# Kernel tuning notes

Measured on AMD Instinct MI355X. Metric: run time of the kernel, lower is better.

Reference implementation:

```python
import jax, jax.numpy as jnp
import numpy as np

NUM_NODES = 100000
EMBED_DIM = 64
NUM_LAYERS = 3
NUM_EDGES = 1250000


def setup_inputs() -> dict:
    key = jax.random.key(0)
    k1, k2 = jax.random.split(key)
    edge_index = jax.random.randint(k1, (2, NUM_EDGES), 0, NUM_NODES, dtype=jnp.int64)
    emb_weight = jax.random.normal(k2, (NUM_NODES, EMBED_DIM), dtype=jnp.float32)
    alpha = jnp.full((NUM_LAYERS + 1,), 1.0 / (NUM_LAYERS + 1), dtype=jnp.float32)
    return {"edge_index": edge_index, "emb_weight": emb_weight, "alpha": alpha}


def reference(edge_index, emb_weight, alpha):
    # edge_index: [2, E] int; emb_weight: [N, d]; alpha: [L+1]
    row, col = edge_index[0], edge_index[1]  # source, target (flow source_to_target)
    N = emb_weight.shape[0]

    # gcn_norm without self-loops: deg over target index, symmetric normalization
    deg = jax.ops.segment_sum(jnp.ones_like(row, dtype=emb_weight.dtype), col, num_segments=N)
    dis = jnp.where(deg > 0, jax.lax.rsqrt(jnp.maximum(deg, 1.0)), 0.0)
    w = dis[row] * dis[col]  # [E]

    x = emb_weight
    out = x * alpha[0]
    for i in range(NUM_LAYERS):
        # gather-scale-scatter: out[col] += w * x[row]
        msg = x[row] * w[:, None]  # [E, d]
        x = jax.ops.segment_sum(msg, col, num_segments=N)
        out = out + x * alpha[i + 1]

    # edge_label_index defaults to edge_index -> dot-product ranking per edge
    return jnp.sum(out[row] * out[col], axis=-1)  # [E]
```

## Files before the change

kernel.cpp:

```cpp
#include <hip/hip_runtime.h>

#define EDIM 64
#define CHUNK 4096
#define BSH 9
#define BCOLS 512
#define CAP 8192

__device__ __forceinline__ unsigned f2_to_bf2(float a, float b) {
    unsigned ua = __float_as_uint(a); ua += 0x7fffu + ((ua >> 16) & 1u);
    unsigned ub = __float_as_uint(b); ub += 0x7fffu + ((ub >> 16) & 1u);
    return (ua >> 16) | (ub & 0xffff0000u);
}
__device__ __forceinline__ float bf_lo(unsigned u) { return __uint_as_float(u << 16); }
__device__ __forceinline__ float bf_hi(unsigned u) { return __uint_as_float(u & 0xffff0000u); }

__global__ void k_binit(int* __restrict__ bcur, int nb) {
    int b = threadIdx.x;
    if (b < nb) bcur[b] = b * CAP;
}

__global__ __launch_bounds__(256) void k_binA(const int* __restrict__ row, const int* __restrict__ col,
                                              int* __restrict__ bcur, uint2* __restrict__ pairs,
                                              int E, int nb) {
    __shared__ uint2 buf[CHUNK];
    __shared__ int histL[256], baseL[256], curL[256], gbaseL[256];
    __shared__ int wsum[4];
    int tid = threadIdx.x;
    int c0 = blockIdx.x * CHUNK;
    int cend = min(CHUNK, E - c0);

    histL[tid] = 0;
    __syncthreads();

    int myr[CHUNK / 256], myc[CHUNK / 256];
    #pragma unroll
    for (int k = 0; k < CHUNK / 256; ++k) {
        int i = k * 256 + tid;
        if (i < cend) {
            int e = c0 + i;
            myr[k] = row[e]; myc[k] = col[e];
            atomicAdd(&histL[myc[k] >> BSH], 1);
        }
    }
    __syncthreads();

    int v = histL[tid];
    int lane = tid & 63, w = tid >> 6;
    int inc = v;
    #pragma unroll
    for (int d = 1; d < 64; d <<= 1) { int t = __shfl_up(inc, d, 64); if (lane >= d) inc += t; }
    if (lane == 63) wsum[w] = inc;
    __syncthreads();
    int woff = 0;
    for (int i = 0; i < w; ++i) woff += wsum[i];
    int excl = inc - v + woff;
    baseL[tid] = excl;
    curL[tid] = excl;
    if (tid < nb) gbaseL[tid] = atomicAdd(&bcur[tid], v);
    __syncthreads();

    #pragma unroll
    for (int k = 0; k < CHUNK / 256; ++k) {
        int i = k * 256 + tid;
        if (i < cend) {
            int b = myc[k] >> BSH;
            int e = c0 + i;
            int pos = atomicAdd(&curL[b], 1);
            buf[pos] = make_uint2((unsigned)myr[k] | ((unsigned)b << 24),
                                  ((unsigned)e << 9) | ((unsigned)myc[k] & (BCOLS - 1)));
        }
    }
    __syncthreads();

    for (int i = tid; i < cend; i += 256) {
        uint2 p = buf[i];
        int b = (int)(p.x >> 24);
        int dst = gbaseL[b] + (i - baseL[b]);
        pairs[dst] = make_uint2(p.x & 0x00FFFFFFu, p.y);
    }
}

__global__ void k_bscan(const int* __restrict__ bcur, int* __restrict__ bbase, int nb) {
    __shared__ int wsum[4];
    int tid = threadIdx.x;
    int v = (tid < nb) ? (bcur[tid] - tid * CAP) : 0;
    int lane = tid & 63, w = tid >> 6;
    int inc = v;
    #pragma unroll
    for (int d = 1; d < 64; d <<= 1) { int t = __shfl_up(inc, d, 64); if (lane >= d) inc += t; }
    if (lane == 63) wsum[w] = inc;
    __syncthreads();
    int woff = 0;
    for (int i = 0; i < w; ++i) woff += wsum[i];
    if (tid < nb) bbase[tid] = inc - v + woff;
}

__global__ __launch_bounds__(256) void k_binB(const uint2* __restrict__ pairs,
                                              const int* __restrict__ bcur, const int* __restrict__ bbase,
                                              int* __restrict__ off, float* __restrict__ dis,
                                              float* __restrict__ invd,
                                              int* __restrict__ rowp, int* __restrict__ eidx, int N) {
    __shared__ int degL[BCOLS];
    __shared__ int curL[BCOLS];
    __shared__ int wsum[4];
    int tid = threadIdx.x;
    int b = blockIdx.x;
    int base_in = b * CAP;
    int cnt = bcur[b] - base_in;
    int col0 = b << BSH;
    int ncols = min(BCOLS, N - col0);

    degL[tid] = 0; degL[tid + 256] = 0;
    __syncthreads();

    for (int i = tid; i < cnt; i += 256)
        atomicAdd(&degL[(int)(pairs[base_in + i].y & (BCOLS - 1))], 1);
    __syncthreads();

    int d0 = degL[2 * tid], d1 = degL[2 * tid + 1];
    int v = d0 + d1;
    int lane = tid & 63, w = tid >> 6;
    int inc = v;
    #pragma unroll
    for (int d = 1; d < 64; d <<= 1) { int t = __shfl_up(inc, d, 64); if (lane >= d) inc += t; }
    if (lane == 63) wsum[w] = inc;
    __syncthreads();
    int woff = 0;
    for (int i = 0; i < w; ++i) woff += wsum[i];
    int exclp = inc - v + woff + bbase[b];
    __syncthreads();
    int c0i = 2 * tid, c1i = 2 * tid + 1;
    if (c0i < ncols) {
        off[col0 + c0i] = exclp;
        dis[col0 + c0i] = (d0 > 0) ? rsqrtf((float)d0) : 0.0f;
        invd[col0 + c0i] = (d0 > 0) ? sqrtf((float)d0) : 0.0f;
        curL[c0i] = exclp;
    }
    if (c1i < ncols) {
        off[col0 + c1i] = exclp + d0;
        dis[col0 + c1i] = (d1 > 0) ? rsqrtf((float)d1) : 0.0f;
        invd[col0 + c1i] = (d1 > 0) ? sqrtf((float)d1) : 0.0f;
        curL[c1i] = exclp + d0;
    }
    __syncthreads();

    for (int i = tid; i < cnt; i += 256) {
        uint2 p = pairs[base_in + i];
        int pos = atomicAdd(&curL[(int)(p.y & (BCOLS - 1))], 1);
        rowp[pos] = (int)p.x;
        eidx[pos] = (int)(p.y >> 9);
    }
}

__global__ __launch_bounds__(256) void k_cvty(const float* __restrict__ emb,
                                              const float* __restrict__ dis,
                                              unsigned* __restrict__ y0, int n16) {
    int i = blockIdx.x * blockDim.x + threadIdx.x;
    if (i < n16) {
        float d = dis[i >> 4];
        float4 v = ((const float4*)emb)[i];
        uint2 o; o.x = f2_to_bf2(d * v.x, d * v.y); o.y = f2_to_bf2(d * v.z, d * v.w);
        ((uint2*)y0)[i] = o;
    }
}

__global__ __launch_bounds__(256) void k_prop(const int* __restrict__ off, const int* __restrict__ rowp,
                                              const float* __restrict__ dis, const float* __restrict__ invd,
                                              const unsigned short* __restrict__ yin,
                                              unsigned short* __restrict__ yout,
                                              const float* __restrict__ emb,
                                              const unsigned short* __restrict__ y1,
                                              const unsigned short* __restrict__ y2,
                                              const float* __restrict__ alpha,
                                              unsigned short* __restrict__ out16,
                                              int N, int E, int last) {
    int t = blockIdx.x * blockDim.x + threadIdx.x;
    int wid = t >> 4;
    if (wid >= N) return;
    int q = threadIdx.x & 15;
    int j0 = off[wid];
    int j1 = (wid == N - 1) ? E : off[wid + 1];
    float ax = 0.0f, ay = 0.0f, az = 0.0f, aw = 0.0f;

    int j = j0;
    for (; j + 3 < j1; j += 4) {
        int r0 = rowp[j], r1 = rowp[j + 1], r2 = rowp[j + 2], r3 = rowp[j + 3];
        uint2 v0 = *(const uint2*)(yin + ((size_t)r0 << 6) + (q << 2));
        uint2 v1 = *(const uint2*)(yin + ((size_t)r1 << 6) + (q << 2));
        uint2 v2 = *(const uint2*)(yin + ((size_t)r2 << 6) + (q << 2));
        uint2 v3 = *(const uint2*)(yin + ((size_t)r3 << 6) + (q << 2));
        ax += bf_lo(v0.x) + bf_lo(v1.x) + bf_lo(v2.x) + bf_lo(v3.x);
        ay += bf_hi(v0.x) + bf_hi(v1.x) + bf_hi(v2.x) + bf_hi(v3.x);
        az += bf_lo(v0.y) + bf_lo(v1.y) + bf_lo(v2.y) + bf_lo(v3.y);
        aw += bf_hi(v0.y) + bf_hi(v1.y) + bf_hi(v2.y) + bf_hi(v3.y);
    }
    for (; j < j1; ++j) {
        int r = rowp[j];
        uint2 v = *(const uint2*)(yin + ((size_t)r << 6) + (q << 2));
        ax += bf_lo(v.x); ay += bf_hi(v.x);
        az += bf_lo(v.y); aw += bf_hi(v.y);
    }

    float d = dis[wid];
    size_t oi = ((size_t)wid << 6) + (q << 2);
    if (!last) {
        float sc = d * d;
        *(uint2*)(yout + oi) = make_uint2(f2_to_bf2(sc * ax, sc * ay),
                                          f2_to_bf2(sc * az, sc * aw));
    } else {
        float iv = invd[wid];
        float a0 = alpha[0], a1 = alpha[1], a2 = alpha[2], a3 = alpha[3];
        float4 e = *(const float4*)(emb + oi);
        uint2 u1 = *(const uint2*)(y1 + oi);
        uint2 u2 = *(const uint2*)(y2 + oi);
        float ox = a0 * e.x + iv * (a1 * bf_lo(u1.x) + a2 * bf_lo(u2.x)) + a3 * d * ax;
        float oy = a0 * e.y + iv * (a1 * bf_hi(u1.x) + a2 * bf_hi(u2.x)) + a3 * d * ay;
        float oz = a0 * e.z + iv * (a1 * bf_lo(u1.y) + a2 * bf_lo(u2.y)) + a3 * d * az;
        float ow = a0 * e.w + iv * (a1 * bf_hi(u1.y) + a2 * bf_hi(u2.y)) + a3 * d * aw;
        *(uint2*)(out16 + oi) = make_uint2(f2_to_bf2(ox, oy), f2_to_bf2(oz, ow));
    }
}

__global__ __launch_bounds__(256) void k_dotc(const int* __restrict__ off, const int* __restrict__ rowp,
                                              const int* __restrict__ eidx,
                                              const unsigned short* __restrict__ out16,
                                              float* __restrict__ res, int N, int E) {
    int t = blockIdx.x * blockDim.x + threadIdx.x;
    int wid = t >> 3;
    if (wid >= N) return;
    int q = threadIdx.x & 7;
    int j0 = off[wid];
    int j1 = (wid == N - 1) ? E : off[wid + 1];

    uint4 bv = *(const uint4*)(out16 + ((size_t)wid << 6) + (q << 3));

    int j = j0;
    for (; j + 3 < j1; j += 4) {
        int r0 = rowp[j],     e0 = eidx[j];
        int r1 = rowp[j + 1], e1 = eidx[j + 1];
        int r2 = rowp[j + 2], e2 = eidx[j + 2];
        int r3 = rowp[j + 3], e3 = eidx[j + 3];
        uint4 a0 = *(const uint4*)(out16 + ((size_t)r0 << 6) + (q << 3));
        uint4 a1 = *(const uint4*)(out16 + ((size_t)r1 << 6) + (q << 3));
        uint4 a2 = *(const uint4*)(out16 + ((size_t)r2 << 6) + (q << 3));
        uint4 a3 = *(const uint4*)(out16 + ((size_t)r3 << 6) + (q << 3));
        float t0 = bf_lo(a0.x) * bf_lo(bv.x) + bf_hi(a0.x) * bf_hi(bv.x)
                 + bf_lo(a0.y) * bf_lo(bv.y) + bf_hi(a0.y) * bf_hi(bv.y)
                 + bf_lo(a0.z) * bf_lo(bv.z) + bf_hi(a0.z) * bf_hi(bv.z)
                 + bf_lo(a0.w) * bf_lo(bv.w) + bf_hi(a0.w) * bf_hi(bv.w);
        float t1 = bf_lo(a1.x) * bf_lo(bv.x) + bf_hi(a1.x) * bf_hi(bv.x)
                 + bf_lo(a1.y) * bf_lo(bv.y) + bf_hi(a1.y) * bf_hi(bv.y)
                 + bf_lo(a1.z) * bf_lo(bv.z) + bf_hi(a1.z) * bf_hi(bv.z)
                 + bf_lo(a1.w) * bf_lo(bv.w) + bf_hi(a1.w) * bf_hi(bv.w);
        float t2 = bf_lo(a2.x) * bf_lo(bv.x) + bf_hi(a2.x) * bf_hi(bv.x)
                 + bf_lo(a2.y) * bf_lo(bv.y) + bf_hi(a2.y) * bf_hi(bv.y)
                 + bf_lo(a2.z) * bf_lo(bv.z) + bf_hi(a2.z) * bf_hi(bv.z)
                 + bf_lo(a2.w) * bf_lo(bv.w) + bf_hi(a2.w) * bf_hi(bv.w);
        float t3 = bf_lo(a3.x) * bf_lo(bv.x) + bf_hi(a3.x) * bf_hi(bv.x)
                 + bf_lo(a3.y) * bf_lo(bv.y) + bf_hi(a3.y) * bf_hi(bv.y)
                 + bf_lo(a3.z) * bf_lo(bv.z) + bf_hi(a3.z) * bf_hi(bv.z)
                 + bf_lo(a3.w) * bf_lo(bv.w) + bf_hi(a3.w) * bf_hi(bv.w);
        t0 += __shfl_xor(t0, 1, 8); t1 += __shfl_xor(t1, 1, 8);
        t2 += __shfl_xor(t2, 1, 8); t3 += __shfl_xor(t3, 1, 8);
        t0 += __shfl_xor(t0, 2, 8); t1 += __shfl_xor(t1, 2, 8);
        t2 += __shfl_xor(t2, 2, 8); t3 += __shfl_xor(t3, 2, 8);
        t0 += __shfl_xor(t0, 4, 8); t1 += __shfl_xor(t1, 4, 8);
        t2 += __shfl_xor(t2, 4, 8); t3 += __shfl_xor(t3, 4, 8);
        if (q == 0) { res[e0] = t0; res[e1] = t1; res[e2] = t2; res[e3] = t3; }
    }
    for (; j < j1; ++j) {
        int r = rowp[j], e = eidx[j];
        uint4 av = *(const uint4*)(out16 + ((size_t)r << 6) + (q << 3));
        float s = bf_lo(av.x) * bf_lo(bv.x) + bf_hi(av.x) * bf_hi(bv.x)
                + bf_lo(av.y) * bf_lo(bv.y) + bf_hi(av.y) * bf_hi(bv.y)
                + bf_lo(av.z) * bf_lo(bv.z) + bf_hi(av.z) * bf_hi(bv.z)
                + bf_lo(av.w) * bf_lo(bv.w) + bf_hi(av.w) * bf_hi(bv.w);
        s += __shfl_xor(s, 1, 8);
        s += __shfl_xor(s, 2, 8);
        s += __shfl_xor(s, 4, 8);
        if (q == 0) res[e] = s;
    }
}

extern "C" void kernel_launch(void* const* d_in, const int* in_sizes, int n_in,
                              void* d_out, int out_size, void* d_ws, size_t ws_size,
                              hipStream_t stream) {
    const int*   edge  = (const int*)d_in[0];
    const float* emb   = (const float*)d_in[1];
    const float* alpha = (const float*)d_in[2];
    float*       res   = (float*)d_out;

    const int E = in_sizes[0] / 2;
    const int N = in_sizes[1] / EDIM;
    const int* row = edge;
    const int* col = edge + E;
    const int NB = (N + BCOLS - 1) >> BSH;

    size_t o = 0;
    int*   offA  = (int*)d_ws + o;   o += (size_t)N;
    float* dis   = (float*)d_ws + o; o += (size_t)N;
    float* invd  = (float*)d_ws + o; o += (size_t)N;
    int*   bcur  = (int*)d_ws + o;   o += 256;
    int*   bbase = (int*)d_ws + o;   o += 256;
    int*   rowp  = (int*)d_ws + o;   o += (size_t)E;
    int*   eidx  = (int*)d_ws + o;   o += (size_t)E;
    unsigned short* y0 = (unsigned short*)((int*)d_ws + o); o += (size_t)N * 32;
    unsigned short* y1 = (unsigned short*)((int*)d_ws + o); o += (size_t)N * 32;
    unsigned short* y2 = (unsigned short*)((int*)d_ws + o); o += (size_t)N * 32;
    uint2* pairs = (uint2*)((int*)d_ws + o);
    unsigned short* out16 = (unsigned short*)pairs;
    (void)ws_size; (void)n_in;

    const int B = 256;
    const int n16 = N * 16;

    k_binit<<<1, 256, 0, stream>>>(bcur, NB);
    k_binA <<<(E + CHUNK - 1) / CHUNK, B, 0, stream>>>(row, col, bcur, pairs, E, NB);
    k_bscan<<<1, 256, 0, stream>>>(bcur, bbase, NB);
    k_binB <<<NB, B, 0, stream>>>(pairs, bcur, bbase, offA, dis, invd, rowp, eidx, N);

    k_cvty <<<(n16 + B - 1) / B, B, 0, stream>>>(emb, dis, (unsigned*)y0, n16);

    k_prop<<<((size_t)N * 16 + B - 1) / B, B, 0, stream>>>(
        offA, rowp, dis, invd, y0, y1, emb, y1, y2, alpha, out16, N, E, 0);
    k_prop<<<((size_t)N * 16 + B - 1) / B, B, 0, stream>>>(
        offA, rowp, dis, invd, y1, y2, emb, y1, y2, alpha, out16, N, E, 0);
    k_prop<<<((size_t)N * 16 + B - 1) / B, B, 0, stream>>>(
        offA, rowp, dis, invd, y2, (unsigned short*)0, emb, y1, y2, alpha, out16, N, E, 1);

    k_dotc<<<((size_t)N * 8 + B - 1) / B, B, 0, stream>>>(offA, rowp, eidx, out16, res, N, E);
}
```

Before: 194.4 us.

## Pad CSR segments to multiples of eight and widen propagation gathers to 16 bytes

Each destination's edge list is padded up to a multiple of eight using dummy entries that point at a zeroed sentinel node row. This removes the scalar tail loops, so the propagate and dot kernels can run a fixed 8-way unrolled gather. Propagation now uses 8 lanes per node with uint4 loads instead of 16 lanes with uint2 loads. The cost is extra padded edges (about three per node on average), more workspace, and the sentinel rows that must be zeroed.

After: 181.3 us. -6.7%, faster.

```diff
diff --git a/kernel.cpp b/kernel.cpp
--- a/kernel.cpp
+++ b/kernel.cpp
@@ -5,6 +5,8 @@
 #define BSH 9
 #define BCOLS 512
 #define CAP 8192
+#define PAD 8
+#define MAXPADB ((PAD - 1) * BCOLS)
 
 __device__ __forceinline__ unsigned f2_to_bf2(float a, float b) {
     unsigned ua = __float_as_uint(a); ua += 0x7fffu + ((ua >> 16) & 1u);
@@ -97,9 +99,10 @@
 
 __global__ __launch_bounds__(256) void k_binB(const uint2* __restrict__ pairs,
                                               const int* __restrict__ bcur, const int* __restrict__ bbase,
-                                              int* __restrict__ off, float* __restrict__ dis,
-                                              float* __restrict__ invd,
-                                              int* __restrict__ rowp, int* __restrict__ eidx, int N) {
+                                              int* __restrict__ offS, int* __restrict__ offE,
+                                              float* __restrict__ dis, float* __restrict__ invd,
+                                              int* __restrict__ rowp, int* __restrict__ eidx,
+                                              int N, int E) {
     __shared__ int degL[BCOLS];
     __shared__ int curL[BCOLS];
     __shared__ int wsum[4];
@@ -109,6 +112,7 @@
     int cnt = bcur[b] - base_in;
     int col0 = b << BSH;
     int ncols = min(BCOLS, N - col0);
+    int Pb = bbase[b] + b * MAXPADB;
 
     degL[tid] = 0; degL[tid + 256] = 0;
     __syncthreads();
@@ -118,7 +122,9 @@
     __syncthreads();
 
     int d0 = degL[2 * tid], d1 = degL[2 * tid + 1];
-    int v = d0 + d1;
+    int p0 = (d0 + PAD - 1) & ~(PAD - 1);
+    int p1 = (d1 + PAD - 1) & ~(PAD - 1);
+    int v = p0 + p1;
     int lane = tid & 63, w = tid >> 6;
     int inc = v;
     #pragma unroll
@@ -127,20 +133,25 @@
     __syncthreads();
     int woff = 0;
     for (int i = 0; i < w; ++i) woff += wsum[i];
-    int exclp = inc - v + woff + bbase[b];
+    int exclp = inc - v + woff + Pb;
     __syncthreads();
     int c0i = 2 * tid, c1i = 2 * tid + 1;
     if (c0i < ncols) {
-        off[col0 + c0i] = exclp;
-        dis[col0 + c0i] = (d0 > 0) ? rsqrtf((float)d0) : 0.0f;
+        offS[col0 + c0i] = exclp;
+        offE[col0 + c0i] = exclp + p0;
+        dis [col0 + c0i] = (d0 > 0) ? rsqrtf((float)d0) : 0.0f;
         invd[col0 + c0i] = (d0 > 0) ? sqrtf((float)d0) : 0.0f;
         curL[c0i] = exclp;
+        for (int k = d0; k < p0; ++k) { rowp[exclp + k] = N; eidx[exclp + k] = E; }
     }
     if (c1i < ncols) {
-        off[col0 + c1i] = exclp + d0;
-        dis[col0 + c1i] = (d1 > 0) ? rsqrtf((float)d1) : 0.0f;
+        int e1 = exclp + p0;
+        offS[col0 + c1i] = e1;
+        offE[col0 + c1i] = e1 + p1;
+        dis [col0 + c1i] = (d1 > 0) ? rsqrtf((float)d1) : 0.0f;
         invd[col0 + c1i] = (d1 > 0) ? sqrtf((float)d1) : 0.0f;
-        curL[c1i] = exclp + d0;
+        curL[c1i] = e1;
+        for (int k = d1; k < p1; ++k) { rowp[e1 + k] = N; eidx[e1 + k] = E; }
     }
     __syncthreads();
 
@@ -154,17 +165,28 @@
 
 __global__ __launch_bounds__(256) void k_cvty(const float* __restrict__ emb,
                                               const float* __restrict__ dis,
-                                              unsigned* __restrict__ y0, int n16) {
+                                              unsigned* __restrict__ y0,
+                                              unsigned* __restrict__ y1,
+                                              unsigned* __restrict__ y2,
+                                              unsigned* __restrict__ o16, int N) {
     int i = blockIdx.x * blockDim.x + threadIdx.x;
+    int n16 = N * 16;
     if (i < n16) {
         float d = dis[i >> 4];
         float4 v = ((const float4*)emb)[i];
         uint2 o; o.x = f2_to_bf2(d * v.x, d * v.y); o.y = f2_to_bf2(d * v.z, d * v.w);
         ((uint2*)y0)[i] = o;
-    }
-}
-
-__global__ __launch_bounds__(256) void k_prop(const int* __restrict__ off, const int* __restrict__ rowp,
+    } else if (i < n16 + 16) {
+        uint2 z = make_uint2(0u, 0u);
+        ((uint2*)y0)[i] = z;
+        ((uint2*)y1)[i] = z;
+        ((uint2*)y2)[i] = z;
+        ((uint2*)o16)[i] = z;
+    }
+}
+
+__global__ __launch_bounds__(256) void k_prop(const int* __restrict__ offS, const int* __restrict__ offE,
+                                              const int* __restrict__ rowp,
                                               const float* __restrict__ dis, const float* __restrict__ invd,
                                               const unsigned short* __restrict__ yin,
                                               unsigned short* __restrict__ yout,
@@ -173,55 +195,80 @@
                                               const unsigned short* __restrict__ y2,
                                               const float* __restrict__ alpha,
                                               unsigned short* __restrict__ out16,
-                                              int N, int E, int last) {
+                                              int N, int last) {
     int t = blockIdx.x * blockDim.x + threadIdx.x;
-    int wid = t >> 4;
+    int wid = t >> 3;
     if (wid >= N) return;
-    int q = threadIdx.x & 15;
-    int j0 = off[wid];
-    int j1 = (wid == N - 1) ? E : off[wid + 1];
-    float ax = 0.0f, ay = 0.0f, az = 0.0f, aw = 0.0f;
-
-    int j = j0;
-    for (; j + 3 < j1; j += 4) {
-        int r0 = rowp[j], r1 = rowp[j + 1], r2 = rowp[j + 2], r3 = rowp[j + 3];
-        uint2 v0 = *(const uint2*)(yin + ((size_t)r0 << 6) + (q << 2));
-        uint2 v1 = *(const uint2*)(yin + ((size_t)r1 << 6) + (q << 2));
-        uint2 v2 = *(const uint2*)(yin + ((size_t)r2 << 6) + (q << 2));
-        uint2 v3 = *(const uint2*)(yin + ((size_t)r3 << 6) + (q << 2));
-        ax += bf_lo(v0.x) + bf_lo(v1.x) + bf_lo(v2.x) + bf_lo(v3.x);
-        ay += bf_hi(v0.x) + bf_hi(v1.x) + bf_hi(v2.x) + bf_hi(v3.x);
-        az += bf_lo(v0.y) + bf_lo(v1.y) + bf_lo(v2.y) + bf_lo(v3.y);
-        aw += bf_hi(v0.y) + bf_hi(v1.y) + bf_hi(v2.y) + bf_hi(v3.y);
-    }
-    for (; j < j1; ++j) {
-        int r = rowp[j];
-        uint2 v = *(const uint2*)(yin + ((size_t)r << 6) + (q << 2));
-        ax += bf_lo(v.x); ay += bf_hi(v.x);
-        az += bf_lo(v.y); aw += bf_hi(v.y);
+    int q = threadIdx.x & 7;
+    int j0 = offS[wid];
+    int j1 = offE[wid];
+    float s0 = 0.f, s1 = 0.f, s2 = 0.f, s3 = 0.f, s4 = 0.f, s5 = 0.f, s6 = 0.f, s7 = 0.f;
+
+    for (int j = j0; j < j1; j += 8) {
+        int r0 = rowp[j],     r1 = rowp[j + 1], r2 = rowp[j + 2], r3 = rowp[j + 3];
+        int r4 = rowp[j + 4], r5 = rowp[j + 5], r6 = rowp[j + 6], r7 = rowp[j + 7];
+        uint4 v0 = *(const uint4*)(yin + ((size_t)r0 << 6) + (q << 3));
+        uint4 v1 = *(const uint4*)(yin + ((size_t)r1 << 6) + (q << 3));
+        uint4 v2 = *(const uint4*)(yin + ((size_t)r2 << 6) + (q << 3));
+        uint4 v3 = *(const uint4*)(yin + ((size_t)r3 << 6) + (q << 3));
+        uint4 v4 = *(const uint4*)(yin + ((size_t)r4 << 6) + (q << 3));
+        uint4 v5 = *(const uint4*)(yin + ((size_t)r5 << 6) + (q << 3));
+        uint4 v6 = *(const uint4*)(yin + ((size_t)r6 << 6) + (q << 3));
+        uint4 v7 = *(const uint4*)(yin + ((size_t)r7 << 6) + (q << 3));
+        s0 += bf_lo(v0.x) + bf_lo(v1.x) + bf_lo(v2.x) + bf_lo(v3.x)
+            + bf_lo(v4.x) + bf_lo(v5.x) + bf_lo(v6.x) + bf_lo(v7.x);
+        s1 += bf_hi(v0.x) + bf_hi(v1.x) + bf_hi(v2.x) + bf_hi(v3.x)
+            + bf_hi(v4.x) + bf_hi(v5.x) + bf_hi(v6.x) + bf_hi(v7.x);
+        s2 += bf_lo(v0.y) + bf_lo(v1.y) + bf_lo(v2.y) + bf_lo(v3.y)
+            + bf_lo(v4.y) + bf_lo(v5.y) + bf_lo(v6.y) + bf_lo(v7.y);
+        s3 += bf_hi(v0.y) + bf_hi(v1.y) + bf_hi(v2.y) + bf_hi(v3.y)
+            + bf_hi(v4.y) + bf_hi(v5.y) + bf_hi(v6.y) + bf_hi(v7.y);
+        s4 += bf_lo(v0.z) + bf_lo(v1.z) + bf_lo(v2.z) + bf_lo(v3.z)
+            + bf_lo(v4.z) + bf_lo(v5.z) + bf_lo(v6.z) + bf_lo(v7.z);
+        s5 += bf_hi(v0.z) + bf_hi(v1.z) + bf_hi(v2.z) + bf_hi(v3.z)
+            + bf_hi(v4.z) + bf_hi(v5.z) + bf_hi(v6.z) + bf_hi(v7.z);
+        s6 += bf_lo(v0.w) + bf_lo(v1.w) + bf_lo(v2.w) + bf_lo(v3.w)
+            + bf_lo(v4.w) + bf_lo(v5.w) + bf_lo(v6.w) + bf_lo(v7.w);
+        s7 += bf_hi(v0.w) + bf_hi(v1.w) + bf_hi(v2.w) + bf_hi(v3.w)
+            + bf_hi(v4.w) + bf_hi(v5.w) + bf_hi(v6.w) + bf_hi(v7.w);
     }
 
     float d = dis[wid];
-    size_t oi = ((size_t)wid << 6) + (q << 2);
+    size_t oi = ((size_t)wid << 6) + (q << 3);
     if (!last) {
         float sc = d * d;
-        *(uint2*)(yout + oi) = make_uint2(f2_to_bf2(sc * ax, sc * ay),
-                                          f2_to_bf2(sc * az, sc * aw));
+        uint4 o;
+        o.x = f2_to_bf2(sc * s0, sc * s1);
+        o.y = f2_to_bf2(sc * s2, sc * s3);
+        o.z = f2_to_bf2(sc * s4, sc * s5);
+        o.w = f2_to_bf2(sc * s6, sc * s7);
+        *(uint4*)(yout + oi) = o;
     } else {
         float iv = invd[wid];
         float a0 = alpha[0], a1 = alpha[1], a2 = alpha[2], a3 = alpha[3];
-        float4 e = *(const float4*)(emb + oi);
-        uint2 u1 = *(const uint2*)(y1 + oi);
-        uint2 u2 = *(const uint2*)(y2 + oi);
-        float ox = a0 * e.x + iv * (a1 * bf_lo(u1.x) + a2 * bf_lo(u2.x)) + a3 * d * ax;
-        float oy = a0 * e.y + iv * (a1 * bf_hi(u1.x) + a2 * bf_hi(u2.x)) + a3 * d * ay;
-        float oz = a0 * e.z + iv * (a1 * bf_lo(u1.y) + a2 * bf_lo(u2.y)) + a3 * d * az;
-        float ow = a0 * e.w + iv * (a1 * bf_hi(u1.y) + a2 * bf_hi(u2.y)) + a3 * d * aw;
-        *(uint2*)(out16 + oi) = make_uint2(f2_to_bf2(ox, oy), f2_to_bf2(oz, ow));
-    }
-}
-
-__global__ __launch_bounds__(256) void k_dotc(const int* __restrict__ off, const int* __restrict__ rowp,
+        float4 ea = *(const float4*)(emb + oi);
+        float4 eb = *(const float4*)(emb + oi + 4);
+        uint4 u1 = *(const uint4*)(y1 + oi);
+        uint4 u2 = *(const uint4*)(y2 + oi);
+        float o0 = a0 * ea.x + iv * (a1 * bf_lo(u1.x) + a2 * bf_lo(u2.x)) + a3 * d * s0;
+        float o1 = a0 * ea.y + iv * (a1 * bf_hi(u1.x) + a2 * bf_hi(u2.x)) + a3 * d * s1;
+        float o2 = a0 * ea.z + iv * (a1 * bf_lo(u1.y) + a2 * bf_lo(u2.y)) + a3 * d * s2;
+        float o3 = a0 * ea.w + iv * (a1 * bf_hi(u1.y) + a2 * bf_hi(u2.y)) + a3 * d * s3;
+        float o4 = a0 * eb.x + iv * (a1 * bf_lo(u1.z) + a2 * bf_lo(u2.z)) + a3 * d * s4;
+        float o5 = a0 * eb.y + iv * (a1 * bf_hi(u1.z) + a2 * bf_hi(u2.z)) + a3 * d * s5;
+        float o6 = a0 * eb.z + iv * (a1 * bf_lo(u1.w) + a2 * bf_lo(u2.w)) + a3 * d * s6;
+        float o7 = a0 * eb.w + iv * (a1 * bf_hi(u1.w) + a2 * bf_hi(u2.w)) + a3 * d * s7;
+        uint4 o;
+        o.x = f2_to_bf2(o0, o1);
+        o.y = f2_to_bf2(o2, o3);
+        o.z = f2_to_bf2(o4, o5);
+        o.w = f2_to_bf2(o6, o7);
+        *(uint4*)(out16 + oi) = o;
+    }
+}
+
+__global__ __launch_bounds__(256) void k_dotc(const int* __restrict__ offS, const int* __restrict__ offE,
+                                              const int* __restrict__ rowp,
                                               const int* __restrict__ eidx,
                                               const unsigned short* __restrict__ out16,
                                               float* __restrict__ res, int N, int E) {
@@ -229,56 +276,53 @@
     int wid = t >> 3;
     if (wid >= N) return;
     int q = threadIdx.x & 7;
-    int j0 = off[wid];
-    int j1 = (wid == N - 1) ? E : off[wid + 1];
+    int j0 = offS[wid];
+    int j1 = offE[wid];
 
     uint4 bv = *(const uint4*)(out16 + ((size_t)wid << 6) + (q << 3));
 
-    int j = j0;
-    for (; j + 3 < j1; j += 4) {
-        int r0 = rowp[j],     e0 = eidx[j];
-        int r1 = rowp[j + 1], e1 = eidx[j + 1];
-        int r2 = rowp[j + 2], e2 = eidx[j + 2];
-        int r3 = rowp[j + 3], e3 = eidx[j + 3];
+    for (int j = j0; j < j1; j += 8) {
+        int r0 = rowp[j],     r1 = rowp[j + 1], r2 = rowp[j + 2], r3 = rowp[j + 3];
+        int r4 = rowp[j + 4], r5 = rowp[j + 5], r6 = rowp[j + 6], r7 = rowp[j + 7];
         uint4 a0 = *(const uint4*)(out16 + ((size_t)r0 << 6) + (q << 3));
         uint4 a1 = *(const uint4*)(out16 + ((size_t)r1 << 6) + (q << 3));
         uint4 a2 = *(const uint4*)(out16 + ((size_t)r2 << 6) + (q << 3));
         uint4 a3 = *(const uint4*)(out16 + ((size_t)r3 << 6) + (q << 3));
-        float t0 = bf_lo(a0.x) * bf_lo(bv.x) + bf_hi(a0.x) * bf_hi(bv.x)
-                 + bf_lo(a0.y) * bf_lo(bv.y) + bf_hi(a0.y) * bf_hi(bv.y)
-                 + bf_lo(a0.z) * bf_lo(bv.z) + bf_hi(a0.z) * bf_hi(bv.z)
-                 + bf_lo(a0.w) * bf_lo(bv.w) + bf_hi(a0.w) * bf_hi(bv.w);
-        float t1 = bf_lo(a1.x) * bf_lo(bv.x) + bf_hi(a1.x) * bf_hi(bv.x)
-                 + bf_lo(a1.y) * bf_lo(bv.y) + bf_hi(a1.y) * bf_hi(bv.y)
-                 + bf_lo(a1.z) * bf_lo(bv.z) + bf_hi(a1.z) * bf_hi(bv.z)
-                 + bf_lo(a1.w) * bf_lo(bv.w) + bf_hi(a1.w) * bf_hi(bv.w);
-        float t2 = bf_lo(a2.x) * bf_lo(bv.x) + bf_hi(a2.x) * bf_hi(bv.x)
-                 + bf_lo(a2.y) * bf_lo(bv.y) + bf_hi(a2.y) * bf_hi(bv.y)
-                 + bf_lo(a2.z) * bf_lo(bv.z) + bf_hi(a2.z) * bf_hi(bv.z)
-                 + bf_lo(a2.w) * bf_lo(bv.w) + bf_hi(a2.w) * bf_hi(bv.w);
-        float t3 = bf_lo(a3.x) * bf_lo(bv.x) + bf_hi(a3.x) * bf_hi(bv.x)
-                 + bf_lo(a3.y) * bf_lo(bv.y) + bf_hi(a3.y) * bf_hi(bv.y)
-                 + bf_lo(a3.z) * bf_lo(bv.z) + bf_hi(a3.z) * bf_hi(bv.z)
-                 + bf_lo(a3.w) * bf_lo(bv.w) + bf_hi(a3.w) * bf_hi(bv.w);
+        uint4 a4 = *(const uint4*)(out16 + ((size_t)r4 << 6) + (q << 3));
+        uint4 a5 = *(const uint4*)(out16 + ((size_t)r5 << 6) + (q << 3));
+        uint4 a6 = *(const uint4*)(out16 + ((size_t)r6 << 6) + (q << 3));
+        uint4 a7 = *(const uint4*)(out16 + ((size_t)r7 << 6) + (q << 3));
+        #define DOT8(av) (bf_lo(av.x)*bf_lo(bv.x) + bf_hi(av.x)*bf_hi(bv.x) \
+                        + bf_lo(av.y)*bf_lo(bv.y) + bf_hi(av.y)*bf_hi(bv.y) \
+                        + bf_lo(av.z)*bf_lo(bv.z) + bf_hi(av.z)*bf_hi(bv.z) \
+                        + bf_lo(av.w)*bf_lo(bv.w) + bf_hi(av.w)*bf_hi(bv.w))
+        float t0 = DOT8(a0), t1 = DOT8(a1), t2 = DOT8(a2), t3 = DOT8(a3);
+        float t4 = DOT8(a4), t5 = DOT8(a5), t6 = DOT8(a6), t7 = DOT8(a7);
+        #undef DOT8
         t0 += __shfl_xor(t0, 1, 8); t1 += __shfl_xor(t1, 1, 8);
         t2 += __shfl_xor(t2, 1, 8); t3 += __shfl_xor(t3, 1, 8);
+        t4 += __shfl_xor(t4, 1, 8); t5 += __shfl_xor(t5, 1, 8);
+        t6 += __shfl_xor(t6, 1, 8); t7 += __shfl_xor(t7, 1, 8);
         t0 += __shfl_xor(t0, 2, 8); t1 += __shfl_xor(t1, 2, 8);
         t2 += __shfl_xor(t2, 2, 8); t3 += __shfl_xor(t3, 2, 8);
+        t4 += __shfl_xor(t4, 2, 8); t5 += __shfl_xor(t5, 2, 8);
+        t6 += __shfl_xor(t6, 2, 8); t7 += __shfl_xor(t7, 2, 8);
         t0 += __shfl_xor(t0, 4, 8); t1 += __shfl_xor(t1, 4, 8);
         t2 += __shfl_xor(t2, 4, 8); t3 += __shfl_xor(t3, 4, 8);
-        if (q == 0) { res[e0] = t0; res[e1] = t1; res[e2] = t2; res[e3] = t3; }
-    }
-    for (; j < j1; ++j) {
-        int r = rowp[j], e = eidx[j];
-        uint4 av = *(const uint4*)(out16 + ((size_t)r << 6) + (q << 3));
-        float s = bf_lo(av.x) * bf_lo(bv.x) + bf_hi(av.x) * bf_hi(bv.x)
-                + bf_lo(av.y) * bf_lo(bv.y) + bf_hi(av.y) * bf_hi(bv.y)
-                + bf_lo(av.z) * bf_lo(bv.z) + bf_hi(av.z) * bf_hi(bv.z)
-                + bf_lo(av.w) * bf_lo(bv.w) + bf_hi(av.w) * bf_hi(bv.w);
-        s += __shfl_xor(s, 1, 8);
-        s += __shfl_xor(s, 2, 8);
-        s += __shfl_xor(s, 4, 8);
-        if (q == 0) res[e] = s;
+        t4 += __shfl_xor(t4, 4, 8); t5 += __shfl_xor(t5, 4, 8);
+        t6 += __shfl_xor(t6, 4, 8); t7 += __shfl_xor(t7, 4, 8);
+        if (q == 0) {
+            int e0 = eidx[j],     e1 = eidx[j + 1], e2 = eidx[j + 2], e3 = eidx[j + 3];
+            int e4 = eidx[j + 4], e5 = eidx[j + 5], e6 = eidx[j + 6], e7 = eidx[j + 7];
+            if (e0 < E) res[e0] = t0;
+            if (e1 < E) res[e1] = t1;
+            if (e2 < E) res[e2] = t2;
+            if (e3 < E) res[e3] = t3;
+            if (e4 < E) res[e4] = t4;
+            if (e5 < E) res[e5] = t5;
+            if (e6 < E) res[e6] = t6;
+            if (e7 < E) res[e7] = t7;
+        }
     }
 }
 
@@ -295,38 +339,41 @@
     const int* row = edge;
     const int* col = edge + E;
     const int NB = (N + BCOLS - 1) >> BSH;
+    const size_t EPAD = (size_t)E + (size_t)NB * MAXPADB + 64;
 
     size_t o = 0;
-    int*   offA  = (int*)d_ws + o;   o += (size_t)N;
+    int*   offS  = (int*)d_ws + o;   o += (size_t)N;
+    int*   offE  = (int*)d_ws + o;   o += (size_t)N;
     float* dis   = (float*)d_ws + o; o += (size_t)N;
     float* invd  = (float*)d_ws + o; o += (size_t)N;
     int*   bcur  = (int*)d_ws + o;   o += 256;
     int*   bbase = (int*)d_ws + o;   o += 256;
-    int*   rowp  = (int*)d_ws + o;   o += (size_t)E;
-    int*   eidx  = (int*)d_ws + o;   o += (size_t)E;
-    unsigned short* y0 = (unsigned short*)((int*)d_ws + o); o += (size_t)N * 32;
-    unsigned short* y1 = (unsigned short*)((int*)d_ws + o); o += (size_t)N * 32;
-    unsigned short* y2 = (unsigned short*)((int*)d_ws + o); o += (size_t)N * 32;
+    int*   rowp  = (int*)d_ws + o;   o += EPAD;
+    int*   eidx  = (int*)d_ws + o;   o += EPAD;
+    unsigned short* y0 = (unsigned short*)((int*)d_ws + o); o += (size_t)(N + 1) * 32;
+    unsigned short* y1 = (unsigned short*)((int*)d_ws + o); o += (size_t)(N + 1) * 32;
+    unsigned short* y2 = (unsigned short*)((int*)d_ws + o); o += (size_t)(N + 1) * 32;
     uint2* pairs = (uint2*)((int*)d_ws + o);
     unsigned short* out16 = (unsigned short*)pairs;
     (void)ws_size; (void)n_in;
 
     const int B = 256;
-    const int n16 = N * 16;
 
     k_binit<<<1, 256, 0, stream>>>(bcur, NB);
     k_binA <<<(E + CHUNK - 1) / CHUNK, B, 0, stream>>>(row, col, bcur, pairs, E, NB);
     k_bscan<<<1, 256, 0, stream>>>(bcur, bbase, NB);
-    k_binB <<<NB, B, 0, stream>>>(pairs, bcur, bbase, offA, dis, invd, rowp, eidx, N);
-
-    k_cvty <<<(n16 + B - 1) / B, B, 0, stream>>>(emb, dis, (unsigned*)y0, n16);
-
-    k_prop<<<((size_t)N * 16 + B - 1) / B, B, 0, stream>>>(
-        offA, rowp, dis, invd, y0, y1, emb, y1, y2, alpha, out16, N, E, 0);
-    k_prop<<<((size_t)N * 16 + B - 1) / B, B, 0, stream>>>(
-        offA, rowp, dis, invd, y1, y2, emb, y1, y2, alpha, out16, N, E, 0);
-    k_prop<<<((size_t)N * 16 + B - 1) / B, B, 0, stream>>>(
-        offA, rowp, dis, invd, y2, (unsigned short*)0, emb, y1, y2, alpha, out16, N, E, 1);
-
-    k_dotc<<<((size_t)N * 8 + B - 1) / B, B, 0, stream>>>(offA, rowp, eidx, out16, res, N, E);
-}
+    k_binB <<<NB, B, 0, stream>>>(pairs, bcur, bbase, offS, offE, dis, invd, rowp, eidx, N, E);
+
+    k_cvty <<<(N * 16 + 16 + B - 1) / B, B, 0, stream>>>(emb, dis, (unsigned*)y0,
+                                                         (unsigned*)y1, (unsigned*)y2,
+                                                         (unsigned*)out16, N);
+
+    k_prop<<<((size_t)N * 8 + B - 1) / B, B, 0, stream>>>(
+        offS, offE, rowp, dis, invd, y0, y1, emb, y1, y2, alpha, out16, N, 0);
+    k_prop<<<((size_t)N * 8 + B - 1) / B, B, 0, stream>>>(
+        offS, offE, rowp, dis, invd, y1, y2, emb, y1, y2, alpha, out16, N, 0);
+    k_prop<<<((size_t)N * 8 + B - 1) / B, B, 0, stream>>>(
+        offS, offE, rowp, dis, invd, y2, (unsigned short*)0, emb, y1, y2, alpha, out16, N, 1);
+
+    k_dotc<<<((size_t)N * 8 + B - 1) / B, B, 0, stream>>>(offS, offE, rowp, eidx, out16, res, N, E);
+}
```
